# Kernel optimization log

Measured on AMD Instinct MI355X. Metric: run time of the kernel, lower is better.

Reference implementation:

```python
import jax, jax.numpy as jnp
import numpy as np

EMBED_DIM = 1024
HEAD_NUM = 16
HEAD_DIM = 64


def setup_inputs() -> dict:
    key = jax.random.key(0)
    ks = jax.random.split(key, 9)
    B, S = 4, 4096
    sc = 1.0 / np.sqrt(HEAD_DIM)
    scf = 1.0 / np.sqrt(HEAD_NUM * HEAD_DIM)
    return {
        "value": jax.random.normal(ks[0], (B, S, EMBED_DIM), jnp.float32),
        "key": jax.random.normal(ks[1], (B, S, EMBED_DIM), jnp.float32),
        "query": jax.random.normal(ks[2], (B, S, EMBED_DIM), jnp.float32),
        "Wv": jax.random.normal(ks[3], (HEAD_DIM, HEAD_DIM), jnp.float32) * sc,
        "bv": jnp.zeros((HEAD_DIM,), jnp.float32),
        "Wk": jax.random.normal(ks[4], (HEAD_DIM, HEAD_DIM), jnp.float32) * sc,
        "bk": jnp.zeros((HEAD_DIM,), jnp.float32),
        "Wq": jax.random.normal(ks[5], (HEAD_DIM, HEAD_DIM), jnp.float32) * sc,
        "bq": jnp.zeros((HEAD_DIM,), jnp.float32),
        "Wfc": jax.random.normal(ks[6], (EMBED_DIM, HEAD_NUM * HEAD_DIM), jnp.float32) * scf,
        "bfc": jnp.zeros((EMBED_DIM,), jnp.float32),
    }


def reference(value, key, query, Wv, bv, Wk, bk, Wq, bq, Wfc, bfc):
    B, S, _ = value.shape
    H, D = HEAD_NUM, HEAD_DIM
    # reshape to [B, S, H, D]; per-head linear shares weights across heads
    v = value.reshape(B, S, H, D) @ Wv.T + bv
    k = key.reshape(B, S, H, D) @ Wk.T + bk
    q = query.reshape(B, S, H, D) @ Wq.T + bq
    # NOTE: faithful to original: attention over HEAD axis per position -> [B,S,H,H]
    energy = jnp.einsum("bshd,bsgd->bshg", q, k)
    attn = jax.nn.softmax(energy / jnp.sqrt(jnp.asarray(D, energy.dtype)), axis=-1)
    out = jnp.einsum("bshg,bsgd->bshd", attn, v).reshape(B, S, H * D)
    return out @ Wfc.T + bfc
```

## Files before the change

kernel.cpp:

```cpp
#include <hip/hip_runtime.h>
#include <hip/hip_bf16.h>

#define AS1 __attribute__((address_space(1)))
#define AS3 __attribute__((address_space(3)))

typedef __attribute__((ext_vector_type(8))) short bf16x8v;
typedef __attribute__((ext_vector_type(4))) short bf16x4v;
typedef __attribute__((ext_vector_type(4))) float f32x4;

#define MFMA32 __builtin_amdgcn_mfma_f32_16x16x32_bf16
#define MFMA16 __builtin_amdgcn_mfma_f32_16x16x16bf16_1k

__device__ __forceinline__ short f2bf(float f) {
  __hip_bfloat16 h = __float2bfloat16(f);
  return *reinterpret_cast<short*>(&h);
}
__device__ __forceinline__ bf16x4v cvt4(f32x4 v) {
  bf16x4v r; r[0]=f2bf(v[0]); r[1]=f2bf(v[1]); r[2]=f2bf(v[2]); r[3]=f2bf(v[3]);
  return r;
}
__device__ __forceinline__ bf16x8v cvt8(float4 a, float4 b) {
  bf16x8v r;
  r[0]=f2bf(a.x); r[1]=f2bf(a.y); r[2]=f2bf(a.z); r[3]=f2bf(a.w);
  r[4]=f2bf(b.x); r[5]=f2bf(b.y); r[6]=f2bf(b.z); r[7]=f2bf(b.w);
  return r;
}

__global__ void prep_kernel(const float* __restrict__ Wq, const float* __restrict__ Wk,
                            const float* __restrict__ Wv, const float* __restrict__ Wfc,
                            __hip_bfloat16* __restrict__ Wqb, __hip_bfloat16* __restrict__ Wkb,
                            __hip_bfloat16* __restrict__ Wvb, __hip_bfloat16* __restrict__ Wfcb)
{
  int i = blockIdx.x * blockDim.x + threadIdx.x;
  if (i < 64 * 64) {
    Wqb[i] = __float2bfloat16(Wq[i]);
    Wkb[i] = __float2bfloat16(Wk[i]);
    Wvb[i] = __float2bfloat16(Wv[i]);
  }
  for (int j = i; j < 1024 * 1024; j += gridDim.x * blockDim.x)
    Wfcb[j] = __float2bfloat16(Wfc[j]);
}

struct TokL {
  float4 qa0, qb0, qa1, qb1;
  float4 ka0, kb0, ka1, kb1;
  float4 va0, vb0, va1, vb1;
};

__global__ __launch_bounds__(256, 2) void attn_kernel(
    const float* __restrict__ Vin, const float* __restrict__ Kin,
    const float* __restrict__ Qin,
    const __hip_bfloat16* __restrict__ Wvb, const __hip_bfloat16* __restrict__ Wkb,
    const __hip_bfloat16* __restrict__ Wqb,
    const float* __restrict__ bv, const float* __restrict__ bk,
    const float* __restrict__ bq,
    __hip_bfloat16* __restrict__ Xout)
{
  const int wid = threadIdx.x >> 6, lane = threadIdx.x & 63;
  const int lo = lane & 15, hi = lane >> 4;
  const int tok0 = (blockIdx.x * 4 + wid) * 4;
  const int xoff = lo * 64 + hi * 8;

  bf16x8v wqf[4][2], wkf[4][2], wvf[4][2];
#pragma unroll
  for (int i = 0; i < 4; ++i)
#pragma unroll
    for (int ks = 0; ks < 2; ++ks) {
      const int off = (i * 16 + lo) * 64 + ks * 32 + hi * 8;
      wqf[i][ks] = *(const bf16x8v*)(Wqb + off);
      wkf[i][ks] = *(const bf16x8v*)(Wkb + off);
      wvf[i][ks] = *(const bf16x8v*)(Wvb + off);
    }
  float4 bq4[4], bk4[4]; float bvv[4];
#pragma unroll
  for (int i = 0; i < 4; ++i) {
    bq4[i] = *(const float4*)(bq + i * 16 + hi * 4);
    bk4[i] = *(const float4*)(bk + i * 16 + hi * 4);
    bvv[i] = bv[i * 16 + lo];
  }

  auto load_tok = [&](int tl, TokL& L) {
    const size_t tb = (size_t)(tok0 + tl) * 1024;
    const float* qp = Qin + tb + xoff;
    const float* kp = Kin + tb + xoff;
    const float* vp = Vin + tb + xoff;
    L.qa0 = *(const float4*)(qp);      L.qb0 = *(const float4*)(qp + 4);
    L.qa1 = *(const float4*)(qp + 32); L.qb1 = *(const float4*)(qp + 36);
    L.ka0 = *(const float4*)(kp);      L.kb0 = *(const float4*)(kp + 4);
    L.ka1 = *(const float4*)(kp + 32); L.kb1 = *(const float4*)(kp + 36);
    L.va0 = *(const float4*)(vp);      L.vb0 = *(const float4*)(vp + 4);
    L.va1 = *(const float4*)(vp + 32); L.vb1 = *(const float4*)(vp + 36);
  };

  auto compute_tok = [&](int tl, const TokL& L) {
    const size_t tb = (size_t)(tok0 + tl) * 1024;
    bf16x8v xq0 = cvt8(L.qa0, L.qb0), xq1 = cvt8(L.qa1, L.qb1);
    bf16x8v xk0 = cvt8(L.ka0, L.kb0), xk1 = cvt8(L.ka1, L.kb1);

    f32x4 qt[4], kt[4];
#pragma unroll
    for (int i = 0; i < 4; ++i) {
      f32x4 aq = { bq4[i].x, bq4[i].y, bq4[i].z, bq4[i].w };
      aq = MFMA32(wqf[i][0], xq0, aq, 0, 0, 0);
      aq = MFMA32(wqf[i][1], xq1, aq, 0, 0, 0);
      qt[i] = aq;
      f32x4 ak = { bk4[i].x, bk4[i].y, bk4[i].z, bk4[i].w };
      ak = MFMA32(wkf[i][0], xk0, ak, 0, 0, 0);
      ak = MFMA32(wkf[i][1], xk1, ak, 0, 0, 0);
      kt[i] = ak;
    }

    f32x4 ea = { 0.f, 0.f, 0.f, 0.f }, eb = { 0.f, 0.f, 0.f, 0.f };
    ea = MFMA16(cvt4(kt[0]), cvt4(qt[0]), ea, 0, 0, 0);
    eb = MFMA16(cvt4(kt[1]), cvt4(qt[1]), eb, 0, 0, 0);
    ea = MFMA16(cvt4(kt[2]), cvt4(qt[2]), ea, 0, 0, 0);
    eb = MFMA16(cvt4(kt[3]), cvt4(qt[3]), eb, 0, 0, 0);
    f32x4 e = ea + eb;

    float mx = fmaxf(fmaxf(e[0], e[1]), fmaxf(e[2], e[3]));
    mx = fmaxf(mx, __shfl_xor(mx, 16));
    mx = fmaxf(mx, __shfl_xor(mx, 32));
    float p0 = __expf((e[0] - mx) * 0.125f);
    float p1 = __expf((e[1] - mx) * 0.125f);
    float p2 = __expf((e[2] - mx) * 0.125f);
    float p3 = __expf((e[3] - mx) * 0.125f);
    float s = p0 + p1 + p2 + p3;
    s += __shfl_xor(s, 16);
    s += __shfl_xor(s, 32);
    const float inv = 1.0f / s;
    bf16x4v pa;
    pa[0] = f2bf(p0 * inv); pa[1] = f2bf(p1 * inv);
    pa[2] = f2bf(p2 * inv); pa[3] = f2bf(p3 * inv);

    bf16x8v xv0 = cvt8(L.va0, L.vb0), xv1 = cvt8(L.va1, L.vb1);
    f32x4 vc[4];
#pragma unroll
    for (int i = 0; i < 4; ++i) {
      f32x4 av = { bvv[i], bvv[i], bvv[i], bvv[i] };
      av = MFMA32(xv0, wvf[i][0], av, 0, 0, 0);
      av = MFMA32(xv1, wvf[i][1], av, 0, 0, 0);
      vc[i] = av;
    }

    __hip_bfloat16* xo = Xout + tb + (size_t)hi * 4 * 64 + lo;
#pragma unroll
    for (int ni = 0; ni < 4; ++ni) {
      f32x4 z = { 0.f, 0.f, 0.f, 0.f };
      z = MFMA16(pa, cvt4(vc[ni]), z, 0, 0, 0);
#pragma unroll
      for (int j = 0; j < 4; ++j)
        xo[j * 64 + ni * 16] = __float2bfloat16(z[j]);
    }
  };

  TokL A, B;
  load_tok(0, A);
  load_tok(1, B);
  compute_tok(0, A);
  load_tok(2, A);
  compute_tok(1, B);
  load_tok(3, B);
  compute_tok(2, A);
  compute_tok(3, B);
}

__global__ __launch_bounds__(256) void gemm_kernel(
    const __hip_bfloat16* __restrict__ A,
    const __hip_bfloat16* __restrict__ B,
    const float* __restrict__ bias, float* __restrict__ C)
{
  constexpr int K = 1024, N = 1024;
  __shared__ __hip_bfloat16 Asm[128 * 64];
  __shared__ __hip_bfloat16 Bsm[128 * 64];
  const int tid = threadIdx.x, wid = tid >> 6, lane = tid & 63;
  const int bm = blockIdx.x >> 3, bn = blockIdx.x & 7;
  const int m0 = bm * 128, n0 = bn * 128;
  const int wr = wid >> 1, wc = wid & 1;

  f32x4 acc[4][4];
#pragma unroll
  for (int i = 0; i < 4; ++i)
#pragma unroll
    for (int j = 0; j < 4; ++j) acc[i][j] = (f32x4){0.f, 0.f, 0.f, 0.f};

  const int lrow = lane >> 3;
  const int gcol = ((lane & 7) ^ lrow) * 8;

  for (int kt = 0; kt < K / 64; ++kt) {
    const int k0 = kt * 64;
    __syncthreads();
#pragma unroll
    for (int c = 0; c < 4; ++c) {
      const int ca = wid * 4 + c;
      const int row = ca * 8 + lrow;
      __builtin_amdgcn_global_load_lds(
          (const AS1 void*)(A + (size_t)(m0 + row) * K + k0 + gcol),
          (AS3 void*)((char*)Asm + ca * 1024), 16, 0, 0);
      __builtin_amdgcn_global_load_lds(
          (const AS1 void*)(B + (size_t)(n0 + row) * K + k0 + gcol),
          (AS3 void*)((char*)Bsm + ca * 1024), 16, 0, 0);
    }
    asm volatile("s_waitcnt vmcnt(0)" ::: "memory");
    __syncthreads();

#pragma unroll
    for (int ks = 0; ks < 2; ++ks) {
      bf16x8v af[4], bfr[4];
#pragma unroll
      for (int mi = 0; mi < 4; ++mi) {
        const int arow = wr * 64 + mi * 16 + (lane & 15);
        const int slot = (ks * 4 + (lane >> 4)) ^ (arow & 7);
        af[mi] = *(const bf16x8v*)((const char*)Asm + arow * 128 + slot * 16);
      }
#pragma unroll
      for (int ni = 0; ni < 4; ++ni) {
        const int brow = wc * 64 + ni * 16 + (lane & 15);
        const int slot = (ks * 4 + (lane >> 4)) ^ (brow & 7);
        bfr[ni] = *(const bf16x8v*)((const char*)Bsm + brow * 128 + slot * 16);
      }
#pragma unroll
      for (int mi = 0; mi < 4; ++mi)
#pragma unroll
        for (int ni = 0; ni < 4; ++ni)
          acc[mi][ni] = __builtin_amdgcn_mfma_f32_16x16x32_bf16(
              af[mi], bfr[ni], acc[mi][ni], 0, 0, 0);
    }
  }

#pragma unroll
  for (int mi = 0; mi < 4; ++mi) {
    const int r0 = m0 + wr * 64 + mi * 16 + (lane >> 4) * 4;
#pragma unroll
    for (int ni = 0; ni < 4; ++ni) {
      const int c = n0 + wc * 64 + ni * 16 + (lane & 15);
      const float bs = bias[c];
#pragma unroll
      for (int j = 0; j < 4; ++j)
        C[(size_t)(r0 + j) * N + c] = acc[mi][ni][j] + bs;
    }
  }
}

extern "C" void kernel_launch(void* const* d_in, const int* in_sizes, int n_in,
                              void* d_out, int out_size, void* d_ws, size_t ws_size,
                              hipStream_t stream)
{
  const float* value = (const float*)d_in[0];
  const float* key   = (const float*)d_in[1];
  const float* query = (const float*)d_in[2];
  const float* Wv  = (const float*)d_in[3];
  const float* bv  = (const float*)d_in[4];
  const float* Wk  = (const float*)d_in[5];
  const float* bk  = (const float*)d_in[6];
  const float* Wq  = (const float*)d_in[7];
  const float* bq  = (const float*)d_in[8];
  const float* Wfc = (const float*)d_in[9];
  const float* bfc = (const float*)d_in[10];
  float* out = (float*)d_out;

  char* ws = (char*)d_ws;
  __hip_bfloat16* Xb   = (__hip_bfloat16*)ws;
  __hip_bfloat16* Wfcb = (__hip_bfloat16*)(ws + 33554432);
  __hip_bfloat16* Wqb  = (__hip_bfloat16*)(ws + 33554432 + 2097152);
  __hip_bfloat16* Wkb  = Wqb + 4096;
  __hip_bfloat16* Wvb  = Wkb + 4096;

  prep_kernel<<<4096, 256, 0, stream>>>(Wq, Wk, Wv, Wfc, Wqb, Wkb, Wvb, Wfcb);
  attn_kernel<<<1024, 256, 0, stream>>>(value, key, query, Wvb, Wkb, Wqb,
                                        bv, bk, bq, Xb);
  gemm_kernel<<<1024, 256, 0, stream>>>(Xb, Wfcb, bfc, out);
}
```

Before: 116.6 us.

## Stage Q/K through LDS with async global_load_lds double buffering in attention kernel

The attention kernel now gives each wave 8 tokens instead of 4. Q and K rows are streamed into a per-wave double-buffered LDS region with global_load_lds, under manual vmcnt/lgkmcnt waits. V is prefetched into registers one token ahead, and the grid is halved to match. The GEMM block index mapping is also swapped so consecutive blocks walk M rather than N, which changes L2 reuse of weight tiles. The aim is to hide global load latency and cut register pressure. The cost is fragile hand-written waitcnt counts, 64KB of LDS per block, and fewer blocks in flight.

Result: faster. 109.6 us (-6.0%).

```diff
diff --git a/kernel.cpp b/kernel.cpp
--- a/kernel.cpp
+++ b/kernel.cpp
@@ -41,13 +41,9 @@
     Wfcb[j] = __float2bfloat16(Wfc[j]);
 }
 
-struct TokL {
-  float4 qa0, qb0, qa1, qb1;
-  float4 ka0, kb0, ka1, kb1;
-  float4 va0, vb0, va1, vb1;
-};
-
-__global__ __launch_bounds__(256, 2) void attn_kernel(
+struct TokV { float4 va0, vb0, va1, vb1; float4 va2, vb2, va3, vb3; float4 va4, vb4, va5, vb5; };
+
+__global__ __launch_bounds__(256) void attn_kernel(
     const float* __restrict__ Vin, const float* __restrict__ Kin,
     const float* __restrict__ Qin,
     const __hip_bfloat16* __restrict__ Wvb, const __hip_bfloat16* __restrict__ Wkb,
@@ -56,10 +52,12 @@
     const float* __restrict__ bq,
     __hip_bfloat16* __restrict__ Xout)
 {
+  __shared__ float lds[4][2][2048];
   const int wid = threadIdx.x >> 6, lane = threadIdx.x & 63;
   const int lo = lane & 15, hi = lane >> 4;
-  const int tok0 = (blockIdx.x * 4 + wid) * 4;
-  const int xoff = lo * 64 + hi * 8;
+  constexpr int NT = 8;
+  const int tok0 = (blockIdx.x * 4 + wid) * NT;
+  const int fo = lo * 64 + hi * 8;
 
   bf16x8v wqf[4][2], wkf[4][2], wvf[4][2];
 #pragma unroll
@@ -79,23 +77,53 @@
     bvv[i] = bv[i * 16 + lo];
   }
 
-  auto load_tok = [&](int tl, TokL& L) {
-    const size_t tb = (size_t)(tok0 + tl) * 1024;
-    const float* qp = Qin + tb + xoff;
-    const float* kp = Kin + tb + xoff;
-    const float* vp = Vin + tb + xoff;
-    L.qa0 = *(const float4*)(qp);      L.qb0 = *(const float4*)(qp + 4);
-    L.qa1 = *(const float4*)(qp + 32); L.qb1 = *(const float4*)(qp + 36);
-    L.ka0 = *(const float4*)(kp);      L.kb0 = *(const float4*)(kp + 4);
-    L.ka1 = *(const float4*)(kp + 32); L.kb1 = *(const float4*)(kp + 36);
-    L.va0 = *(const float4*)(vp);      L.vb0 = *(const float4*)(vp + 4);
-    L.va1 = *(const float4*)(vp + 32); L.vb1 = *(const float4*)(vp + 36);
+  auto stageQK = [&](int n) {
+    const size_t tb = (size_t)(tok0 + n) * 1024;
+    float* dq = &lds[wid][n & 1][0];
+    float* dk = &lds[wid][n & 1][1024];
+    const float* gq = Qin + tb + lane * 4;
+    const float* gk = Kin + tb + lane * 4;
+#pragma unroll
+    for (int i = 0; i < 4; ++i)
+      __builtin_amdgcn_global_load_lds((const AS1 void*)(gq + i * 256),
+                                       (AS3 void*)(dq + i * 256), 16, 0, 0);
+#pragma unroll
+    for (int i = 0; i < 4; ++i)
+      __builtin_amdgcn_global_load_lds((const AS1 void*)(gk + i * 256),
+                                       (AS3 void*)(dk + i * 256), 16, 0, 0);
   };
 
-  auto compute_tok = [&](int tl, const TokL& L) {
-    const size_t tb = (size_t)(tok0 + tl) * 1024;
-    bf16x8v xq0 = cvt8(L.qa0, L.qb0), xq1 = cvt8(L.qa1, L.qb1);
-    bf16x8v xk0 = cvt8(L.ka0, L.kb0), xk1 = cvt8(L.ka1, L.kb1);
+  auto loadV = [&](int n, TokV& T) {
+    const float* vp = Vin + (size_t)(tok0 + n) * 1024 + fo;
+    T.va0 = *(const float4*)(vp);      T.vb0 = *(const float4*)(vp + 4);
+    T.va1 = *(const float4*)(vp + 32); T.vb1 = *(const float4*)(vp + 36);
+    T.va2 = T.va0; T.vb2 = T.vb0; T.va3 = T.va1; T.vb3 = T.vb1;
+    T.va4 = T.va0; T.vb4 = T.vb0; T.va5 = T.va1; T.vb5 = T.vb1;
+  };
+
+  stageQK(0);
+  stageQK(1);
+  TokV V;
+  {
+    const float* vp = Vin + (size_t)tok0 * 1024 + fo;
+    V.va0 = *(const float4*)(vp);      V.vb0 = *(const float4*)(vp + 4);
+    V.va1 = *(const float4*)(vp + 32); V.vb1 = *(const float4*)(vp + 36);
+  }
+
+#pragma unroll
+  for (int n = 0; n < NT; ++n) {
+    if (n < NT - 1) { asm volatile("s_waitcnt vmcnt(20)" ::: "memory"); }
+    else           { asm volatile("s_waitcnt vmcnt(12)" ::: "memory"); }
+    __builtin_amdgcn_sched_barrier(0);
+
+    const float* qs = &lds[wid][n & 1][0];
+    const float* ksrc = &lds[wid][n & 1][1024];
+    float4 qa0 = *(const float4*)(qs + fo),      qb0 = *(const float4*)(qs + fo + 4);
+    float4 qa1 = *(const float4*)(qs + fo + 32), qb1 = *(const float4*)(qs + fo + 36);
+    float4 ka0 = *(const float4*)(ksrc + fo),      kb0 = *(const float4*)(ksrc + fo + 4);
+    float4 ka1 = *(const float4*)(ksrc + fo + 32), kb1 = *(const float4*)(ksrc + fo + 36);
+    bf16x8v xq0 = cvt8(qa0, qb0), xq1 = cvt8(qa1, qb1);
+    bf16x8v xk0 = cvt8(ka0, kb0), xk1 = cvt8(ka1, kb1);
 
     f32x4 qt[4], kt[4];
 #pragma unroll
@@ -132,7 +160,7 @@
     pa[0] = f2bf(p0 * inv); pa[1] = f2bf(p1 * inv);
     pa[2] = f2bf(p2 * inv); pa[3] = f2bf(p3 * inv);
 
-    bf16x8v xv0 = cvt8(L.va0, L.vb0), xv1 = cvt8(L.va1, L.vb1);
+    bf16x8v xv0 = cvt8(V.va0, V.vb0), xv1 = cvt8(V.va1, V.vb1);
     f32x4 vc[4];
 #pragma unroll
     for (int i = 0; i < 4; ++i) {
@@ -142,7 +170,7 @@
       vc[i] = av;
     }
 
-    __hip_bfloat16* xo = Xout + tb + (size_t)hi * 4 * 64 + lo;
+    __hip_bfloat16* xo = Xout + (size_t)(tok0 + n) * 1024 + (size_t)hi * 4 * 64 + lo;
 #pragma unroll
     for (int ni = 0; ni < 4; ++ni) {
       f32x4 z = { 0.f, 0.f, 0.f, 0.f };
@@ -151,17 +179,21 @@
       for (int j = 0; j < 4; ++j)
         xo[j * 64 + ni * 16] = __float2bfloat16(z[j]);
     }
-  };
-
-  TokL A, B;
-  load_tok(0, A);
-  load_tok(1, B);
-  compute_tok(0, A);
-  load_tok(2, A);
-  compute_tok(1, B);
-  load_tok(3, B);
-  compute_tok(2, A);
-  compute_tok(3, B);
+
+    asm volatile("" ::: "memory");
+    if (n + 1 < NT) {
+      const float* vp = Vin + (size_t)(tok0 + n + 1) * 1024 + fo;
+      V.va0 = *(const float4*)(vp);      V.vb0 = *(const float4*)(vp + 4);
+      V.va1 = *(const float4*)(vp + 32); V.vb1 = *(const float4*)(vp + 36);
+    }
+    asm volatile("" ::: "memory");
+    if (n + 2 < NT) {
+      asm volatile("s_waitcnt lgkmcnt(0)" ::: "memory");
+      __builtin_amdgcn_sched_barrier(0);
+      stageQK(n + 2);
+    }
+    asm volatile("" ::: "memory");
+  }
 }
 
 __global__ __launch_bounds__(256) void gemm_kernel(
@@ -173,7 +205,7 @@
   __shared__ __hip_bfloat16 Asm[128 * 64];
   __shared__ __hip_bfloat16 Bsm[128 * 64];
   const int tid = threadIdx.x, wid = tid >> 6, lane = tid & 63;
-  const int bm = blockIdx.x >> 3, bn = blockIdx.x & 7;
+  const int bm = blockIdx.x & 127, bn = blockIdx.x >> 7;
   const int m0 = bm * 128, n0 = bn * 128;
   const int wr = wid >> 1, wc = wid & 1;
 
@@ -266,7 +298,7 @@
   __hip_bfloat16* Wvb  = Wkb + 4096;
 
   prep_kernel<<<4096, 256, 0, stream>>>(Wq, Wk, Wv, Wfc, Wqb, Wkb, Wvb, Wfcb);
-  attn_kernel<<<1024, 256, 0, stream>>>(value, key, query, Wvb, Wkb, Wqb,
-                                        bv, bk, bq, Xb);
+  attn_kernel<<<512, 256, 0, stream>>>(value, key, query, Wvb, Wkb, Wqb,
+                                       bv, bk, bq, Xb);
   gemm_kernel<<<1024, 256, 0, stream>>>(Xb, Wfcb, bfc, out);
 }
```

## Fuse per-head attention and output projection into one kernel via LDS staging

Applied to the files above, without the earlier changes.

Merges the attention kernel and the output GEMM into a single kernel. Each block processes 32 tokens, writes the bf16 attention output into swizzled shared memory, then multiplies it by Wfc, which is pre-permuted into an MFMA-fragment-friendly layout so the B operand can be read directly from global memory without LDS. This removes the 32 MB intermediate write and read of X and one kernel launch. In exchange, each block re-reads the full 2 MB Wfc (512 blocks, served mostly from cache), uses 64 KB of LDS per block, and holds many accumulator registers, which limits occupancy.

New measurement: 297.0 us. 155% more time.

```diff
diff --git a/kernel.cpp b/kernel.cpp
--- a/kernel.cpp
+++ b/kernel.cpp
@@ -29,7 +29,7 @@
 __global__ void prep_kernel(const float* __restrict__ Wq, const float* __restrict__ Wk,
                             const float* __restrict__ Wv, const float* __restrict__ Wfc,
                             __hip_bfloat16* __restrict__ Wqb, __hip_bfloat16* __restrict__ Wkb,
-                            __hip_bfloat16* __restrict__ Wvb, __hip_bfloat16* __restrict__ Wfcb)
+                            __hip_bfloat16* __restrict__ Wvb, __hip_bfloat16* __restrict__ Wfcf)
 {
   int i = blockIdx.x * blockDim.x + threadIdx.x;
   if (i < 64 * 64) {
@@ -37,8 +37,12 @@
     Wkb[i] = __float2bfloat16(Wk[i]);
     Wvb[i] = __float2bfloat16(Wv[i]);
   }
-  for (int j = i; j < 1024 * 1024; j += gridDim.x * blockDim.x)
-    Wfcb[j] = __float2bfloat16(Wfc[j]);
+  for (int j = i; j < 1024 * 1024; j += gridDim.x * blockDim.x) {
+    const int r = j >> 10, c = j & 1023;
+    const int dst = (((r >> 4) * 32 + (c >> 5)) * 512) +
+                    ((((c >> 3) & 3) * 16 + (r & 15)) * 8) + (c & 7);
+    Wfcf[dst] = __float2bfloat16(Wfc[j]);
+  }
 }
 
 struct TokL {
@@ -47,196 +51,179 @@
   float4 va0, vb0, va1, vb1;
 };
 
-__global__ __launch_bounds__(256, 2) void attn_kernel(
+__global__ __launch_bounds__(256) void fused_kernel(
     const float* __restrict__ Vin, const float* __restrict__ Kin,
     const float* __restrict__ Qin,
     const __hip_bfloat16* __restrict__ Wvb, const __hip_bfloat16* __restrict__ Wkb,
     const __hip_bfloat16* __restrict__ Wqb,
     const float* __restrict__ bv, const float* __restrict__ bk,
     const float* __restrict__ bq,
-    __hip_bfloat16* __restrict__ Xout)
+    const __hip_bfloat16* __restrict__ Wfcf, const float* __restrict__ bfc,
+    float* __restrict__ out)
 {
+  __shared__ __hip_bfloat16 Xs[32 * 1024];
+  char* xchar = (char*)Xs;
   const int wid = threadIdx.x >> 6, lane = threadIdx.x & 63;
   const int lo = lane & 15, hi = lane >> 4;
-  const int tok0 = (blockIdx.x * 4 + wid) * 4;
+  const int tokb = blockIdx.x * 32;
+  const int t0 = wid * 8;
   const int xoff = lo * 64 + hi * 8;
 
-  bf16x8v wqf[4][2], wkf[4][2], wvf[4][2];
-#pragma unroll
-  for (int i = 0; i < 4; ++i)
-#pragma unroll
-    for (int ks = 0; ks < 2; ++ks) {
-      const int off = (i * 16 + lo) * 64 + ks * 32 + hi * 8;
-      wqf[i][ks] = *(const bf16x8v*)(Wqb + off);
-      wkf[i][ks] = *(const bf16x8v*)(Wkb + off);
-      wvf[i][ks] = *(const bf16x8v*)(Wvb + off);
-    }
-  float4 bq4[4], bk4[4]; float bvv[4];
-#pragma unroll
-  for (int i = 0; i < 4; ++i) {
-    bq4[i] = *(const float4*)(bq + i * 16 + hi * 4);
-    bk4[i] = *(const float4*)(bk + i * 16 + hi * 4);
-    bvv[i] = bv[i * 16 + lo];
-  }
-
-  auto load_tok = [&](int tl, TokL& L) {
-    const size_t tb = (size_t)(tok0 + tl) * 1024;
-    const float* qp = Qin + tb + xoff;
-    const float* kp = Kin + tb + xoff;
-    const float* vp = Vin + tb + xoff;
-    L.qa0 = *(const float4*)(qp);      L.qb0 = *(const float4*)(qp + 4);
-    L.qa1 = *(const float4*)(qp + 32); L.qb1 = *(const float4*)(qp + 36);
-    L.ka0 = *(const float4*)(kp);      L.kb0 = *(const float4*)(kp + 4);
-    L.ka1 = *(const float4*)(kp + 32); L.kb1 = *(const float4*)(kp + 36);
-    L.va0 = *(const float4*)(vp);      L.vb0 = *(const float4*)(vp + 4);
-    L.va1 = *(const float4*)(vp + 32); L.vb1 = *(const float4*)(vp + 36);
-  };
-
-  auto compute_tok = [&](int tl, const TokL& L) {
-    const size_t tb = (size_t)(tok0 + tl) * 1024;
-    bf16x8v xq0 = cvt8(L.qa0, L.qb0), xq1 = cvt8(L.qa1, L.qb1);
-    bf16x8v xk0 = cvt8(L.ka0, L.kb0), xk1 = cvt8(L.ka1, L.kb1);
-
-    f32x4 qt[4], kt[4];
+  {
+    bf16x8v wqf[4][2], wkf[4][2], wvf[4][2];
+#pragma unroll
+    for (int i = 0; i < 4; ++i)
+#pragma unroll
+      for (int ks = 0; ks < 2; ++ks) {
+        const int off = (i * 16 + lo) * 64 + ks * 32 + hi * 8;
+        wqf[i][ks] = *(const bf16x8v*)(Wqb + off);
+        wkf[i][ks] = *(const bf16x8v*)(Wkb + off);
+        wvf[i][ks] = *(const bf16x8v*)(Wvb + off);
+      }
+    float4 bq4[4], bk4[4]; float bvv[4];
 #pragma unroll
     for (int i = 0; i < 4; ++i) {
-      f32x4 aq = { bq4[i].x, bq4[i].y, bq4[i].z, bq4[i].w };
-      aq = MFMA32(wqf[i][0], xq0, aq, 0, 0, 0);
-      aq = MFMA32(wqf[i][1], xq1, aq, 0, 0, 0);
-      qt[i] = aq;
-      f32x4 ak = { bk4[i].x, bk4[i].y, bk4[i].z, bk4[i].w };
-      ak = MFMA32(wkf[i][0], xk0, ak, 0, 0, 0);
-      ak = MFMA32(wkf[i][1], xk1, ak, 0, 0, 0);
-      kt[i] = ak;
-    }
-
-    f32x4 ea = { 0.f, 0.f, 0.f, 0.f }, eb = { 0.f, 0.f, 0.f, 0.f };
-    ea = MFMA16(cvt4(kt[0]), cvt4(qt[0]), ea, 0, 0, 0);
-    eb = MFMA16(cvt4(kt[1]), cvt4(qt[1]), eb, 0, 0, 0);
-    ea = MFMA16(cvt4(kt[2]), cvt4(qt[2]), ea, 0, 0, 0);
-    eb = MFMA16(cvt4(kt[3]), cvt4(qt[3]), eb, 0, 0, 0);
-    f32x4 e = ea + eb;
-
-    float mx = fmaxf(fmaxf(e[0], e[1]), fmaxf(e[2], e[3]));
-    mx = fmaxf(mx, __shfl_xor(mx, 16));
-    mx = fmaxf(mx, __shfl_xor(mx, 32));
-    float p0 = __expf((e[0] - mx) * 0.125f);
-    float p1 = __expf((e[1] - mx) * 0.125f);
-    float p2 = __expf((e[2] - mx) * 0.125f);
-    float p3 = __expf((e[3] - mx) * 0.125f);
-    float s = p0 + p1 + p2 + p3;
-    s += __shfl_xor(s, 16);
-    s += __shfl_xor(s, 32);
-    const float inv = 1.0f / s;
-    bf16x4v pa;
-    pa[0] = f2bf(p0 * inv); pa[1] = f2bf(p1 * inv);
-    pa[2] = f2bf(p2 * inv); pa[3] = f2bf(p3 * inv);
-
-    bf16x8v xv0 = cvt8(L.va0, L.vb0), xv1 = cvt8(L.va1, L.vb1);
-    f32x4 vc[4];
-#pragma unroll
-    for (int i = 0; i < 4; ++i) {
-      f32x4 av = { bvv[i], bvv[i], bvv[i], bvv[i] };
-      av = MFMA32(xv0, wvf[i][0], av, 0, 0, 0);
-      av = MFMA32(xv1, wvf[i][1], av, 0, 0, 0);
-      vc[i] = av;
-    }
-
-    __hip_bfloat16* xo = Xout + tb + (size_t)hi * 4 * 64 + lo;
-#pragma unroll
-    for (int ni = 0; ni < 4; ++ni) {
-      f32x4 z = { 0.f, 0.f, 0.f, 0.f };
-      z = MFMA16(pa, cvt4(vc[ni]), z, 0, 0, 0);
-#pragma unroll
-      for (int j = 0; j < 4; ++j)
-        xo[j * 64 + ni * 16] = __float2bfloat16(z[j]);
-    }
-  };
-
-  TokL A, B;
-  load_tok(0, A);
-  load_tok(1, B);
-  compute_tok(0, A);
-  load_tok(2, A);
-  compute_tok(1, B);
-  load_tok(3, B);
-  compute_tok(2, A);
-  compute_tok(3, B);
-}
-
-__global__ __launch_bounds__(256) void gemm_kernel(
-    const __hip_bfloat16* __restrict__ A,
-    const __hip_bfloat16* __restrict__ B,
-    const float* __restrict__ bias, float* __restrict__ C)
-{
-  constexpr int K = 1024, N = 1024;
-  __shared__ __hip_bfloat16 Asm[128 * 64];
-  __shared__ __hip_bfloat16 Bsm[128 * 64];
-  const int tid = threadIdx.x, wid = tid >> 6, lane = tid & 63;
-  const int bm = blockIdx.x >> 3, bn = blockIdx.x & 7;
-  const int m0 = bm * 128, n0 = bn * 128;
-  const int wr = wid >> 1, wc = wid & 1;
-
-  f32x4 acc[4][4];
-#pragma unroll
-  for (int i = 0; i < 4; ++i)
-#pragma unroll
-    for (int j = 0; j < 4; ++j) acc[i][j] = (f32x4){0.f, 0.f, 0.f, 0.f};
-
-  const int lrow = lane >> 3;
-  const int gcol = ((lane & 7) ^ lrow) * 8;
-
-  for (int kt = 0; kt < K / 64; ++kt) {
-    const int k0 = kt * 64;
-    __syncthreads();
-#pragma unroll
-    for (int c = 0; c < 4; ++c) {
-      const int ca = wid * 4 + c;
-      const int row = ca * 8 + lrow;
-      __builtin_amdgcn_global_load_lds(
-          (const AS1 void*)(A + (size_t)(m0 + row) * K + k0 + gcol),
-          (AS3 void*)((char*)Asm + ca * 1024), 16, 0, 0);
-      __builtin_amdgcn_global_load_lds(
-          (const AS1 void*)(B + (size_t)(n0 + row) * K + k0 + gcol),
-          (AS3 void*)((char*)Bsm + ca * 1024), 16, 0, 0);
-    }
-    asm volatile("s_waitcnt vmcnt(0)" ::: "memory");
-    __syncthreads();
-
-#pragma unroll
-    for (int ks = 0; ks < 2; ++ks) {
-      bf16x8v af[4], bfr[4];
-#pragma unroll
-      for (int mi = 0; mi < 4; ++mi) {
-        const int arow = wr * 64 + mi * 16 + (lane & 15);
-        const int slot = (ks * 4 + (lane >> 4)) ^ (arow & 7);
-        af[mi] = *(const bf16x8v*)((const char*)Asm + arow * 128 + slot * 16);
-      }
+      bq4[i] = *(const float4*)(bq + i * 16 + hi * 4);
+      bk4[i] = *(const float4*)(bk + i * 16 + hi * 4);
+      bvv[i] = bv[i * 16 + lo];
+    }
+
+    auto load_tok = [&](int n, TokL& L) {
+      const size_t tb = (size_t)(tokb + t0 + n) * 1024;
+      const float* qp = Qin + tb + xoff;
+      const float* kp = Kin + tb + xoff;
+      const float* vp = Vin + tb + xoff;
+      L.qa0 = *(const float4*)(qp);      L.qb0 = *(const float4*)(qp + 4);
+      L.qa1 = *(const float4*)(qp + 32); L.qb1 = *(const float4*)(qp + 36);
+      L.ka0 = *(const float4*)(kp);      L.kb0 = *(const float4*)(kp + 4);
+      L.ka1 = *(const float4*)(kp + 32); L.kb1 = *(const float4*)(kp + 36);
+      L.va0 = *(const float4*)(vp);      L.vb0 = *(const float4*)(vp + 4);
+      L.va1 = *(const float4*)(vp + 32); L.vb1 = *(const float4*)(vp + 36);
+    };
+
+    auto compute_tok = [&](int n, const TokL& L) {
+      bf16x8v xq0 = cvt8(L.qa0, L.qb0), xq1 = cvt8(L.qa1, L.qb1);
+      bf16x8v xk0 = cvt8(L.ka0, L.kb0), xk1 = cvt8(L.ka1, L.kb1);
+
+      f32x4 qt[4], kt[4];
+#pragma unroll
+      for (int i = 0; i < 4; ++i) {
+        f32x4 aq = { bq4[i].x, bq4[i].y, bq4[i].z, bq4[i].w };
+        aq = MFMA32(wqf[i][0], xq0, aq, 0, 0, 0);
+        aq = MFMA32(wqf[i][1], xq1, aq, 0, 0, 0);
+        qt[i] = aq;
+        f32x4 ak = { bk4[i].x, bk4[i].y, bk4[i].z, bk4[i].w };
+        ak = MFMA32(wkf[i][0], xk0, ak, 0, 0, 0);
+        ak = MFMA32(wkf[i][1], xk1, ak, 0, 0, 0);
+        kt[i] = ak;
+      }
+
+      f32x4 ea = { 0.f, 0.f, 0.f, 0.f }, eb = { 0.f, 0.f, 0.f, 0.f };
+      ea = MFMA16(cvt4(kt[0]), cvt4(qt[0]), ea, 0, 0, 0);
+      eb = MFMA16(cvt4(kt[1]), cvt4(qt[1]), eb, 0, 0, 0);
+      ea = MFMA16(cvt4(kt[2]), cvt4(qt[2]), ea, 0, 0, 0);
+      eb = MFMA16(cvt4(kt[3]), cvt4(qt[3]), eb, 0, 0, 0);
+      f32x4 e = ea + eb;
+
+      float mx = fmaxf(fmaxf(e[0], e[1]), fmaxf(e[2], e[3]));
+      mx = fmaxf(mx, __shfl_xor(mx, 16));
+      mx = fmaxf(mx, __shfl_xor(mx, 32));
+      float p0 = __expf((e[0] - mx) * 0.125f);
+      float p1 = __expf((e[1] - mx) * 0.125f);
+      float p2 = __expf((e[2] - mx) * 0.125f);
+      float p3 = __expf((e[3] - mx) * 0.125f);
+      float s = p0 + p1 + p2 + p3;
+      s += __shfl_xor(s, 16);
+      s += __shfl_xor(s, 32);
+      const float inv = 1.0f / s;
+      bf16x4v pa;
+      pa[0] = f2bf(p0 * inv); pa[1] = f2bf(p1 * inv);
+      pa[2] = f2bf(p2 * inv); pa[3] = f2bf(p3 * inv);
+
+      bf16x8v xv0 = cvt8(L.va0, L.vb0), xv1 = cvt8(L.va1, L.vb1);
+      f32x4 vc[4];
+#pragma unroll
+      for (int i = 0; i < 4; ++i) {
+        f32x4 av = { bvv[i], bvv[i], bvv[i], bvv[i] };
+        av = MFMA32(xv0, wvf[i][0], av, 0, 0, 0);
+        av = MFMA32(xv1, wvf[i][1], av, 0, 0, 0);
+        vc[i] = av;
+      }
+
+      const int tl = t0 + n;
+      const int tb2 = tl * 2048;
+      const int sw = (tl & 7) << 4;
 #pragma unroll
       for (int ni = 0; ni < 4; ++ni) {
-        const int brow = wc * 64 + ni * 16 + (lane & 15);
-        const int slot = (ks * 4 + (lane >> 4)) ^ (brow & 7);
-        bfr[ni] = *(const bf16x8v*)((const char*)Bsm + brow * 128 + slot * 16);
-      }
-#pragma unroll
-      for (int mi = 0; mi < 4; ++mi)
-#pragma unroll
-        for (int ni = 0; ni < 4; ++ni)
-          acc[mi][ni] = __builtin_amdgcn_mfma_f32_16x16x32_bf16(
-              af[mi], bfr[ni], acc[mi][ni], 0, 0, 0);
-    }
-  }
-
-#pragma unroll
-  for (int mi = 0; mi < 4; ++mi) {
-    const int r0 = m0 + wr * 64 + mi * 16 + (lane >> 4) * 4;
-#pragma unroll
-    for (int ni = 0; ni < 4; ++ni) {
-      const int c = n0 + wc * 64 + ni * 16 + (lane & 15);
-      const float bs = bias[c];
-#pragma unroll
-      for (int j = 0; j < 4; ++j)
-        C[(size_t)(r0 + j) * N + c] = acc[mi][ni][j] + bs;
+        f32x4 z = { 0.f, 0.f, 0.f, 0.f };
+        z = MFMA16(pa, cvt4(vc[ni]), z, 0, 0, 0);
+#pragma unroll
+        for (int j = 0; j < 4; ++j) {
+          const int fbyte = ((hi * 4 + j) * 64 + ni * 16 + lo) * 2;
+          *(short*)(xchar + ((tb2 + fbyte) ^ sw)) = f2bf(z[j]);
+        }
+      }
+    };
+
+    TokL A, B;
+    load_tok(0, A);
+    load_tok(1, B);
+    compute_tok(0, A);
+    load_tok(2, A);
+    compute_tok(1, B);
+    load_tok(3, B);
+    compute_tok(2, A);
+    load_tok(4, A);
+    compute_tok(3, B);
+    load_tok(5, B);
+    compute_tok(4, A);
+    load_tok(6, A);
+    compute_tok(5, B);
+    load_tok(7, B);
+    compute_tok(6, A);
+    compute_tok(7, B);
+  }
+
+  __syncthreads();
+
+  {
+    const int wc = wid;
+    float bsv[16];
+#pragma unroll
+    for (int ni = 0; ni < 16; ++ni) bsv[ni] = bfc[wc * 256 + ni * 16 + lo];
+
+    f32x4 acc0[16], acc1[16];
+#pragma unroll
+    for (int ni = 0; ni < 16; ++ni) {
+      acc0[ni] = (f32x4){0.f, 0.f, 0.f, 0.f};
+      acc1[ni] = (f32x4){0.f, 0.f, 0.f, 0.f};
+    }
+
+    const __hip_bfloat16* bp0 = Wfcf + (size_t)(wc * 16) * 32 * 512 + lane * 8;
+
+#pragma unroll 2
+    for (int k0 = 0; k0 < 32; ++k0) {
+      const int kb = k0 * 64 + hi * 16;
+      bf16x8v a0 = *(const bf16x8v*)(xchar + ((lo * 2048 + kb) ^ ((lo & 7) << 4)));
+      bf16x8v a1 = *(const bf16x8v*)(xchar + (((16 + lo) * 2048 + kb) ^ ((lo & 7) << 4)));
+      const __hip_bfloat16* bp = bp0 + k0 * 512;
+#pragma unroll
+      for (int ni = 0; ni < 16; ++ni) {
+        bf16x8v bfrag = *(const bf16x8v*)(bp + (size_t)ni * 32 * 512);
+        acc0[ni] = MFMA32(a0, bfrag, acc0[ni], 0, 0, 0);
+        acc1[ni] = MFMA32(a1, bfrag, acc1[ni], 0, 0, 0);
+      }
+    }
+
+    float* o0 = out + (size_t)(tokb + hi * 4) * 1024 + wc * 256 + lo;
+    float* o1 = out + (size_t)(tokb + 16 + hi * 4) * 1024 + wc * 256 + lo;
+#pragma unroll
+    for (int ni = 0; ni < 16; ++ni) {
+#pragma unroll
+      for (int j = 0; j < 4; ++j) {
+        o0[(size_t)j * 1024 + ni * 16] = acc0[ni][j] + bsv[ni];
+        o1[(size_t)j * 1024 + ni * 16] = acc1[ni][j] + bsv[ni];
+      }
     }
   }
 }
@@ -259,14 +246,12 @@
   float* out = (float*)d_out;
 
   char* ws = (char*)d_ws;
-  __hip_bfloat16* Xb   = (__hip_bfloat16*)ws;
-  __hip_bfloat16* Wfcb = (__hip_bfloat16*)(ws + 33554432);
-  __hip_bfloat16* Wqb  = (__hip_bfloat16*)(ws + 33554432 + 2097152);
+  __hip_bfloat16* Wfcf = (__hip_bfloat16*)ws;
+  __hip_bfloat16* Wqb  = (__hip_bfloat16*)(ws + 2097152);
   __hip_bfloat16* Wkb  = Wqb + 4096;
   __hip_bfloat16* Wvb  = Wkb + 4096;
 
-  prep_kernel<<<4096, 256, 0, stream>>>(Wq, Wk, Wv, Wfc, Wqb, Wkb, Wvb, Wfcb);
-  attn_kernel<<<1024, 256, 0, stream>>>(value, key, query, Wvb, Wkb, Wqb,
-                                        bv, bk, bq, Xb);
-  gemm_kernel<<<1024, 256, 0, stream>>>(Xb, Wfcb, bfc, out);
-}
+  prep_kernel<<<4096, 256, 0, stream>>>(Wq, Wk, Wv, Wfc, Wqb, Wkb, Wvb, Wfcf);
+  fused_kernel<<<512, 256, 0, stream>>>(value, key, query, Wvb, Wkb, Wqb,
+                                        bv, bk, bq, Wfcf, bfc, out);
+}
```
